# Optimization experiments

Hardware: AMD Instinct MI355X
Metric: run time of the kernel (lower is better)

Reference implementation:

```python
import jax, jax.numpy as jnp
import numpy as np
import math

NUM_IN_C = 128      # rep_2d num_c (c_z)
ATT_C = 64          # attention_num_c
NUM_HEADS = 4
B, T, I, J = 1, 4, 256, 256


def setup_inputs() -> dict:
    key = jax.random.key(0)
    ks = jax.random.split(key, 7)
    s = 1.0 / math.sqrt(NUM_IN_C)
    return {
        "z2d": jax.random.normal(ks[0], (B, I, J, NUM_IN_C), dtype=jnp.float32),
        "t2d": jax.random.normal(ks[1], (B, T, I, J, NUM_IN_C), dtype=jnp.float32),
        # nn.Linear weights are [out_features, in_features]; apply as x @ W.T
        "Wq": jax.random.normal(ks[2], (ATT_C * NUM_HEADS, NUM_IN_C), dtype=jnp.float32) * s,
        "Wk": jax.random.normal(ks[3], (ATT_C * NUM_HEADS, NUM_IN_C), dtype=jnp.float32) * s,
        "Wv": jax.random.normal(ks[4], (ATT_C * NUM_HEADS, NUM_IN_C), dtype=jnp.float32) * s,
        "Wo": jax.random.normal(ks[5], (NUM_IN_C, ATT_C * NUM_HEADS), dtype=jnp.float32) * s,
        "bo": jax.random.normal(ks[6], (NUM_IN_C,), dtype=jnp.float32) * 0.02,
    }


def reference(z2d, t2d, Wq, Wk, Wv, Wo, bo):
    # Projections; reshape last dim to (attention_num_c, num_heads) per torch .view
    q = (z2d @ Wq.T).reshape(*z2d.shape[:-1], ATT_C, NUM_HEADS)        # b i j c h
    k = (t2d @ Wk.T).reshape(*t2d.shape[:-1], ATT_C, NUM_HEADS)        # b t i j c h
    v = (t2d @ Wv.T).reshape(*t2d.shape[:-1], ATT_C, NUM_HEADS)        # b t i j c h
    # NOTE: original scales by sqrt(num_in_c), not sqrt(attention_num_c)
    scores = jnp.einsum('bijch,btijch->btijh', q, k) / math.sqrt(NUM_IN_C)
    w = jax.nn.softmax(scores, axis=1)                                  # softmax over template axis t
    out = jnp.einsum('btijh,btijch->bijch', w, v)                       # b i j c h
    out = out.reshape(*out.shape[:-2], ATT_C * NUM_HEADS)               # flatten (c,h)
    return out @ Wo.T + bo
```

## Files before the change

kernel.cpp:

```cpp
#include <hip/hip_runtime.h>


#define PIX 65536

typedef __attribute__((ext_vector_type(8))) short s8v;
typedef __attribute__((ext_vector_type(4))) float f4v;
typedef __attribute__((ext_vector_type(4))) unsigned int u4v;
typedef __attribute__((ext_vector_type(4))) float fl4;

__device__ __forceinline__ unsigned short f2bf(float x) {
    unsigned int u = __float_as_uint(x);
    u = (u + 0x7FFFu + ((u >> 16) & 1u)) >> 16;
    return (unsigned short)u;
}
__device__ __forceinline__ float bf2fs(short v) {
    return __uint_as_float(((unsigned int)(unsigned short)v) << 16);
}

__global__ __launch_bounds__(256) void build_weights(
        const float* __restrict__ Wq, const float* __restrict__ Wk,
        const float* __restrict__ Wv, const float* __restrict__ Wo,
        unsigned short* __restrict__ mcat, unsigned short* __restrict__ pcat) {
    int b = blockIdx.x;
    if (b < 256) {
        int idx = b * 256 + threadIdx.x;
        int n = idx >> 7, k1 = idx & 127;
        int h = n >> 7, k2 = n & 127;
        float s = 0.f;
        #pragma unroll 8
        for (int c = 0; c < 64; c++) {
            int r = c * 4 + h;
            s += Wq[r * 128 + k1] * Wk[r * 128 + k2];
        }
        mcat[idx] = f2bf(s * 0.088388347648318447f);
    } else {
        int idx = (b - 256) * 256 + threadIdx.x;
        int m = idx >> 9, kk = idx & 511;
        int h = kk >> 7, k = kk & 127;
        float s = 0.f;
        #pragma unroll 8
        for (int c = 0; c < 64; c++) {
            int r = c * 4 + h;
            s += Wo[m * 256 + r] * Wv[r * 128 + k];
        }
        pcat[idx] = f2bf(s);
    }
}

#define S_SCR_OFS (512 * 136)
#define S_USH (S_SCR_OFS + 8 * 16 * 72)

__global__ __launch_bounds__(512, 2) void score_kernel(
    const float* __restrict__ z2d, const float* __restrict__ t2d,
    const unsigned short* __restrict__ mcat, float* __restrict__ wbuf) {

    __shared__ unsigned short sm[S_USH];
    const int tid = threadIdx.x;

    #pragma unroll
    for (int i = 0; i < 16; i++) {
        int g8 = i * 512 + tid;
        int row = g8 >> 4, c8 = g8 & 15;
        *(u4v*)&sm[row * 136 + c8 * 8] = *(const u4v*)(mcat + (size_t)g8 * 8);
    }
    __syncthreads();

    const int wv = tid >> 6, lane = tid & 63, quad = lane >> 4, l15 = lane & 15;
    unsigned short* scr = &sm[S_SCR_OFS + wv * (16 * 72)];

    for (int it = 0; it < 2; it++) {
        const int p0 = blockIdx.x * 256 + (wv * 2 + it) * 16;

        s8v za[4];
        {
            const float* zp = z2d + (size_t)(p0 + l15) * 128 + quad * 8;
            #pragma unroll
            for (int ks = 0; ks < 4; ks++) {
                const fl4 d0 = *(const fl4*)(zp + ks * 32);
                const fl4 d1 = *(const fl4*)(zp + ks * 32 + 4);
                s8v a;
                a[0] = (short)f2bf(d0[0]); a[1] = (short)f2bf(d0[1]);
                a[2] = (short)f2bf(d0[2]); a[3] = (short)f2bf(d0[3]);
                a[4] = (short)f2bf(d1[0]); a[5] = (short)f2bf(d1[1]);
                a[6] = (short)f2bf(d1[2]); a[7] = (short)f2bf(d1[3]);
                za[ks] = a;
            }
        }
        s8v atf[4][4];
        #pragma unroll
        for (int t = 0; t < 4; t++) {
            const float* ap = t2d + ((size_t)t * PIX + p0 + l15) * 128 + quad * 8;
            #pragma unroll
            for (int kf = 0; kf < 4; kf++) {
                const fl4 d0 = *(const fl4*)(ap + kf * 32);
                const fl4 d1 = *(const fl4*)(ap + kf * 32 + 4);
                s8v a;
                a[0] = (short)f2bf(d0[0]); a[1] = (short)f2bf(d0[1]);
                a[2] = (short)f2bf(d0[2]); a[3] = (short)f2bf(d0[3]);
                a[4] = (short)f2bf(d1[0]); a[5] = (short)f2bf(d1[1]);
                a[6] = (short)f2bf(d1[2]); a[7] = (short)f2bf(d1[3]);
                atf[t][kf] = a;
            }
        }

        for (int h = 0; h < 4; h++) {
            f4v dac[4];
            #pragma unroll
            for (int t = 0; t < 4; t++) dac[t] = (f4v){0.f, 0.f, 0.f, 0.f};

            #pragma unroll
            for (int ph = 0; ph < 2; ph++) {
                f4v uacc[4];
                #pragma unroll
                for (int c = 0; c < 4; c++) {
                    const int brow = h * 128 + (ph * 4 + c) * 16 + l15;
                    f4v acc = {0.f, 0.f, 0.f, 0.f};
                    #pragma unroll
                    for (int ks = 0; ks < 4; ks++) {
                        const s8v b = *(const s8v*)&sm[brow * 136 + ks * 32 + quad * 8];
                        acc = __builtin_amdgcn_mfma_f32_16x16x32_bf16(za[ks], b, acc, 0, 0, 0);
                    }
                    uacc[c] = acc;
                }
                #pragma unroll
                for (int c = 0; c < 4; c++)
                    #pragma unroll
                    for (int r = 0; r < 4; r++)
                        scr[(quad * 4 + r) * 72 + c * 16 + l15] = f2bf(uacc[c][r]);
                __threadfence_block();
                #pragma unroll
                for (int ks2 = 0; ks2 < 2; ks2++) {
                    const s8v uf = *(const s8v*)&scr[l15 * 72 + ks2 * 32 + quad * 8];
                    const int kf = ph * 2 + ks2;
                    #pragma unroll
                    for (int t = 0; t < 4; t++)
                        dac[t] = __builtin_amdgcn_mfma_f32_16x16x32_bf16(
                            uf, atf[t][kf], dac[t], 0, 0, 0);
                }
                __threadfence_block();
            }
            if ((l15 >> 2) == quad) {
                const int r = l15 & 3;
                float x0 = r == 0 ? dac[0][0] : r == 1 ? dac[0][1] : r == 2 ? dac[0][2] : dac[0][3];
                float x1 = r == 0 ? dac[1][0] : r == 1 ? dac[1][1] : r == 2 ? dac[1][2] : dac[1][3];
                float x2 = r == 0 ? dac[2][0] : r == 1 ? dac[2][1] : r == 2 ? dac[2][2] : dac[2][3];
                float x3 = r == 0 ? dac[3][0] : r == 1 ? dac[3][1] : r == 2 ? dac[3][2] : dac[3][3];
                float mx = fmaxf(fmaxf(x0, x1), fmaxf(x2, x3));
                float e0 = __expf(x0 - mx), e1 = __expf(x1 - mx);
                float e2 = __expf(x2 - mx), e3 = __expf(x3 - mx);
                float inv = 1.f / (e0 + e1 + e2 + e3);
                float* wp = wbuf + (size_t)h * 4 * PIX + p0 + l15;
                wp[0 * PIX] = e0 * inv; wp[1 * PIX] = e1 * inv;
                wp[2 * PIX] = e2 * inv; wp[3 * PIX] = e3 * inv;
            }
        }
    }
}

#define O_USH (128 * 520)

__global__ __launch_bounds__(512, 2) void out_kernel(
    const float* __restrict__ t2d, const unsigned short* __restrict__ pcat,
    const float* __restrict__ wbuf, const float* __restrict__ bo,
    float* __restrict__ out) {

    __shared__ unsigned short sm[O_USH];
    const int tid = threadIdx.x;

    #pragma unroll
    for (int i = 0; i < 16; i++) {
        int g8 = i * 512 + tid;
        int row = g8 >> 6, c8 = g8 & 63;
        *(u4v*)&sm[row * 520 + c8 * 8] = *(const u4v*)(pcat + (size_t)g8 * 8);
    }
    __syncthreads();

    const int wv = tid >> 6, lane = tid & 63, quad = lane >> 4, l15 = lane & 15;
    const int p0 = blockIdx.x * 256 + wv * 32;

    float wgt[4][2][4];
    #pragma unroll
    for (int h = 0; h < 4; h++)
        #pragma unroll
        for (int t = 0; t < 4; t++)
            #pragma unroll
            for (int mt = 0; mt < 2; mt++)
                wgt[t][mt][h] = wbuf[(size_t)(h * 4 + t) * PIX + p0 + mt * 16 + l15];

    f4v acc[2][8];
    #pragma unroll
    for (int mt = 0; mt < 2; mt++)
        #pragma unroll
        for (int ct = 0; ct < 8; ct++) acc[mt][ct] = (f4v){0.f, 0.f, 0.f, 0.f};

    #pragma unroll
    for (int ks = 0; ks < 4; ks++) {
        s8v ab[4][2];
        #pragma unroll
        for (int t = 0; t < 4; t++)
            #pragma unroll
            for (int mt = 0; mt < 2; mt++) {
                const float* ap = t2d + ((size_t)t * PIX + p0 + mt * 16 + l15) * 128
                                  + ks * 32 + quad * 8;
                const fl4 d0 = *(const fl4*)ap;
                const fl4 d1 = *(const fl4*)(ap + 4);
                s8v a;
                a[0] = (short)f2bf(d0[0]); a[1] = (short)f2bf(d0[1]);
                a[2] = (short)f2bf(d0[2]); a[3] = (short)f2bf(d0[3]);
                a[4] = (short)f2bf(d1[0]); a[5] = (short)f2bf(d1[1]);
                a[6] = (short)f2bf(d1[2]); a[7] = (short)f2bf(d1[3]);
                ab[t][mt] = a;
            }
        #pragma unroll
        for (int h = 0; h < 4; h++) {
            s8v af[2];
            #pragma unroll
            for (int mt = 0; mt < 2; mt++) {
                s8v o;
                #pragma unroll
                for (int j = 0; j < 8; j++) {
                    float v = wgt[0][mt][h] * bf2fs(ab[0][mt][j])
                            + wgt[1][mt][h] * bf2fs(ab[1][mt][j])
                            + wgt[2][mt][h] * bf2fs(ab[2][mt][j])
                            + wgt[3][mt][h] * bf2fs(ab[3][mt][j]);
                    o[j] = (short)f2bf(v);
                }
                af[mt] = o;
            }
            #pragma unroll
            for (int ct = 0; ct < 8; ct++) {
                const s8v b = *(const s8v*)&sm[(ct * 16 + l15) * 520
                                               + h * 128 + ks * 32 + quad * 8];
                acc[0][ct] = __builtin_amdgcn_mfma_f32_16x16x32_bf16(af[0], b, acc[0][ct], 0, 0, 0);
                acc[1][ct] = __builtin_amdgcn_mfma_f32_16x16x32_bf16(af[1], b, acc[1][ct], 0, 0, 0);
            }
        }
    }

    #pragma unroll
    for (int ct = 0; ct < 8; ct++) {
        const float bb = bo[ct * 16 + l15];
        #pragma unroll
        for (int mt = 0; mt < 2; mt++)
            #pragma unroll
            for (int r = 0; r < 4; r++)
                out[(size_t)(p0 + mt * 16 + quad * 4 + r) * 128 + ct * 16 + l15]
                    = acc[mt][ct][r] + bb;
    }
}

extern "C" void kernel_launch(void* const* d_in, const int* in_sizes, int n_in,
                              void* d_out, int out_size, void* d_ws, size_t ws_size,
                              hipStream_t stream) {
    const float* z2d = (const float*)d_in[0];
    const float* t2d = (const float*)d_in[1];
    const float* Wq  = (const float*)d_in[2];
    const float* Wk  = (const float*)d_in[3];
    const float* Wv  = (const float*)d_in[4];
    const float* Wo  = (const float*)d_in[5];
    const float* bo  = (const float*)d_in[6];

    unsigned short* mcat = (unsigned short*)d_ws;
    unsigned short* pcat = mcat + 512 * 128;
    float* wbuf = (float*)(pcat + 128 * 512);

    build_weights<<<512, 256, 0, stream>>>(Wq, Wk, Wv, Wo, mcat, pcat);
    score_kernel<<<256, 512, 0, stream>>>(z2d, t2d, mcat, wbuf);
    out_kernel<<<256, 512, 0, stream>>>(t2d, pcat, wbuf, bo, (float*)d_out);
}
```

Before: 277.4 us.

## Replace score second MFMA stage with per-lane dot products and shuffle reduction

```diff
diff --git a/kernel.cpp b/kernel.cpp
--- a/kernel.cpp
+++ b/kernel.cpp
@@ -16,6 +16,24 @@
 __device__ __forceinline__ float bf2fs(short v) {
     return __uint_as_float(((unsigned int)(unsigned short)v) << 16);
 }
+
+__device__ __forceinline__ unsigned int cvtpk(float lo, float hi) {
+    unsigned int r;
+    asm("v_cvt_pk_bf16_f32 %0, %1, %2" : "=v"(r) : "v"(lo), "v"(hi));
+    return r;
+}
+
+__device__ __forceinline__ s8v pack8(fl4 d0, fl4 d1) {
+    union { u4v u; s8v s; } cv;
+    cv.u[0] = cvtpk(d0[0], d0[1]);
+    cv.u[1] = cvtpk(d0[2], d0[3]);
+    cv.u[2] = cvtpk(d1[0], d1[1]);
+    cv.u[3] = cvtpk(d1[2], d1[3]);
+    return cv.s;
+}
+
+__device__ __forceinline__ float bflo(unsigned int u) { return __uint_as_float(u << 16); }
+__device__ __forceinline__ float bfhi(unsigned int u) { return __uint_as_float(u & 0xffff0000u); }
 
 __global__ __launch_bounds__(256) void build_weights(
         const float* __restrict__ Wq, const float* __restrict__ Wk,
@@ -47,8 +65,7 @@
     }
 }
 
-#define S_SCR_OFS (512 * 136)
-#define S_USH (S_SCR_OFS + 8 * 16 * 72)
+#define S_USH (512 * 136)
 
 __global__ __launch_bounds__(512, 2) void score_kernel(
     const float* __restrict__ z2d, const float* __restrict__ t2d,
@@ -66,92 +83,62 @@
     __syncthreads();
 
     const int wv = tid >> 6, lane = tid & 63, quad = lane >> 4, l15 = lane & 15;
-    unsigned short* scr = &sm[S_SCR_OFS + wv * (16 * 72)];
 
     for (int it = 0; it < 2; it++) {
         const int p0 = blockIdx.x * 256 + (wv * 2 + it) * 16;
+        const int p = p0 + l15;
 
         s8v za[4];
         {
-            const float* zp = z2d + (size_t)(p0 + l15) * 128 + quad * 8;
-            #pragma unroll
-            for (int ks = 0; ks < 4; ks++) {
-                const fl4 d0 = *(const fl4*)(zp + ks * 32);
-                const fl4 d1 = *(const fl4*)(zp + ks * 32 + 4);
-                s8v a;
-                a[0] = (short)f2bf(d0[0]); a[1] = (short)f2bf(d0[1]);
-                a[2] = (short)f2bf(d0[2]); a[3] = (short)f2bf(d0[3]);
-                a[4] = (short)f2bf(d1[0]); a[5] = (short)f2bf(d1[1]);
-                a[6] = (short)f2bf(d1[2]); a[7] = (short)f2bf(d1[3]);
-                za[ks] = a;
-            }
-        }
-        s8v atf[4][4];
+            const float* zp = z2d + (size_t)p * 128 + quad * 8;
+            #pragma unroll
+            for (int ks = 0; ks < 4; ks++)
+                za[ks] = pack8(*(const fl4*)(zp + ks * 32), *(const fl4*)(zp + ks * 32 + 4));
+        }
+        unsigned int a2[4][8][2];
         #pragma unroll
         for (int t = 0; t < 4; t++) {
-            const float* ap = t2d + ((size_t)t * PIX + p0 + l15) * 128 + quad * 8;
-            #pragma unroll
-            for (int kf = 0; kf < 4; kf++) {
-                const fl4 d0 = *(const fl4*)(ap + kf * 32);
-                const fl4 d1 = *(const fl4*)(ap + kf * 32 + 4);
-                s8v a;
-                a[0] = (short)f2bf(d0[0]); a[1] = (short)f2bf(d0[1]);
-                a[2] = (short)f2bf(d0[2]); a[3] = (short)f2bf(d0[3]);
-                a[4] = (short)f2bf(d1[0]); a[5] = (short)f2bf(d1[1]);
-                a[6] = (short)f2bf(d1[2]); a[7] = (short)f2bf(d1[3]);
-                atf[t][kf] = a;
-            }
-        }
-
+            const float* ap = t2d + ((size_t)t * PIX + p) * 128 + quad * 4;
+            #pragma unroll
+            for (int cb = 0; cb < 8; cb++) {
+                const fl4 v = *(const fl4*)(ap + cb * 16);
+                a2[t][cb][0] = cvtpk(v[0], v[1]);
+                a2[t][cb][1] = cvtpk(v[2], v[3]);
+            }
+        }
+
+        #pragma unroll
         for (int h = 0; h < 4; h++) {
-            f4v dac[4];
-            #pragma unroll
-            for (int t = 0; t < 4; t++) dac[t] = (f4v){0.f, 0.f, 0.f, 0.f};
-
-            #pragma unroll
-            for (int ph = 0; ph < 2; ph++) {
-                f4v uacc[4];
-                #pragma unroll
-                for (int c = 0; c < 4; c++) {
-                    const int brow = h * 128 + (ph * 4 + c) * 16 + l15;
-                    f4v acc = {0.f, 0.f, 0.f, 0.f};
-                    #pragma unroll
-                    for (int ks = 0; ks < 4; ks++) {
-                        const s8v b = *(const s8v*)&sm[brow * 136 + ks * 32 + quad * 8];
-                        acc = __builtin_amdgcn_mfma_f32_16x16x32_bf16(za[ks], b, acc, 0, 0, 0);
-                    }
-                    uacc[c] = acc;
+            float ps[4] = {0.f, 0.f, 0.f, 0.f};
+            #pragma unroll
+            for (int cb = 0; cb < 8; cb++) {
+                f4v u = {0.f, 0.f, 0.f, 0.f};
+                #pragma unroll
+                for (int ks = 0; ks < 4; ks++) {
+                    const s8v a = *(const s8v*)&sm[(h * 128 + cb * 16 + l15) * 136 +
+                                                   ks * 32 + quad * 8];
+                    u = __builtin_amdgcn_mfma_f32_16x16x32_bf16(a, za[ks], u, 0, 0, 0);
                 }
                 #pragma unroll
-                for (int c = 0; c < 4; c++)
-                    #pragma unroll
-                    for (int r = 0; r < 4; r++)
-                        scr[(quad * 4 + r) * 72 + c * 16 + l15] = f2bf(uacc[c][r]);
-                __threadfence_block();
-                #pragma unroll
-                for (int ks2 = 0; ks2 < 2; ks2++) {
-                    const s8v uf = *(const s8v*)&scr[l15 * 72 + ks2 * 32 + quad * 8];
-                    const int kf = ph * 2 + ks2;
-                    #pragma unroll
-                    for (int t = 0; t < 4; t++)
-                        dac[t] = __builtin_amdgcn_mfma_f32_16x16x32_bf16(
-                            uf, atf[t][kf], dac[t], 0, 0, 0);
+                for (int t = 0; t < 4; t++) {
+                    ps[t] += u[0] * bflo(a2[t][cb][0]) + u[1] * bfhi(a2[t][cb][0])
+                           + u[2] * bflo(a2[t][cb][1]) + u[3] * bfhi(a2[t][cb][1]);
                 }
-                __threadfence_block();
-            }
-            if ((l15 >> 2) == quad) {
-                const int r = l15 & 3;
-                float x0 = r == 0 ? dac[0][0] : r == 1 ? dac[0][1] : r == 2 ? dac[0][2] : dac[0][3];
-                float x1 = r == 0 ? dac[1][0] : r == 1 ? dac[1][1] : r == 2 ? dac[1][2] : dac[1][3];
-                float x2 = r == 0 ? dac[2][0] : r == 1 ? dac[2][1] : r == 2 ? dac[2][2] : dac[2][3];
-                float x3 = r == 0 ? dac[3][0] : r == 1 ? dac[3][1] : r == 2 ? dac[3][2] : dac[3][3];
-                float mx = fmaxf(fmaxf(x0, x1), fmaxf(x2, x3));
-                float e0 = __expf(x0 - mx), e1 = __expf(x1 - mx);
-                float e2 = __expf(x2 - mx), e3 = __expf(x3 - mx);
-                float inv = 1.f / (e0 + e1 + e2 + e3);
-                float* wp = wbuf + (size_t)h * 4 * PIX + p0 + l15;
-                wp[0 * PIX] = e0 * inv; wp[1 * PIX] = e1 * inv;
-                wp[2 * PIX] = e2 * inv; wp[3 * PIX] = e3 * inv;
+            }
+            #pragma unroll
+            for (int t = 0; t < 4; t++) {
+                ps[t] += __shfl_xor(ps[t], 16);
+                ps[t] += __shfl_xor(ps[t], 32);
+            }
+            const float mx = fmaxf(fmaxf(ps[0], ps[1]), fmaxf(ps[2], ps[3]));
+            float e[4], sum = 0.f;
+            #pragma unroll
+            for (int t = 0; t < 4; t++) { e[t] = __expf(ps[t] - mx); sum += e[t]; }
+            const float inv = 1.f / sum;
+            if (quad == 0) {
+                #pragma unroll
+                for (int t = 0; t < 4; t++)
+                    wbuf[(size_t)(h * 4 + t) * PIX + p] = e[t] * inv;
             }
         }
     }
```

Result: no change. 278.0 us (+0.2%).
